# Kernel optimization log

Measured on AMD Instinct MI355X. Metric: run time of the kernel, lower is better.

The kernel has to match this reference:

```python
import jax, jax.numpy as jnp
import numpy as np

D_MODEL = 1024
N_HEADS = 16
DEPTH = D_MODEL // N_HEADS
B, S = 2, 2048


def setup_inputs() -> dict:
    key = jax.random.key(0)
    ks = jax.random.split(key, 11)
    scale = 1.0 / np.sqrt(D_MODEL)
    return {
        "q": jax.random.normal(ks[0], (B, S, D_MODEL), jnp.float32),
        "k": jax.random.normal(ks[1], (B, S, D_MODEL), jnp.float32),
        "v": jax.random.normal(ks[2], (B, S, D_MODEL), jnp.float32),
        "wq": jax.random.normal(ks[3], (D_MODEL, D_MODEL), jnp.float32) * scale,
        "bq": jnp.zeros((D_MODEL,), jnp.float32),
        "wk": jax.random.normal(ks[4], (D_MODEL, D_MODEL), jnp.float32) * scale,
        "bk": jnp.zeros((D_MODEL,), jnp.float32),
        "wv": jax.random.normal(ks[5], (D_MODEL, D_MODEL), jnp.float32) * scale,
        "bv": jnp.zeros((D_MODEL,), jnp.float32),
        "wo": jax.random.normal(ks[6], (D_MODEL, D_MODEL), jnp.float32) * scale,
        "bo": jnp.zeros((D_MODEL,), jnp.float32),
    }


def _mha(q, k, v, wq, bq, wk, bk, wv, bv, wo, bo):
    b, s, _ = q.shape
    # separate QKV projections
    qh = (q @ wq + bq).reshape(b, s, N_HEADS, DEPTH).transpose(0, 2, 1, 3)  # [b,h,s,d]
    kh = (k @ wk + bk).reshape(b, s, N_HEADS, DEPTH).transpose(0, 2, 1, 3)
    vh = (v @ wv + bv).reshape(b, s, N_HEADS, DEPTH).transpose(0, 2, 1, 3)
    # keras.layers.Attention default: UNSCALED dot-product scores, causal mask
    scores = jnp.einsum("bhqd,bhkd->bhqk", qh, kh)  # [b,h,s,s]
    causal = jnp.tril(jnp.ones((s, s), bool))
    scores = jnp.where(causal, scores, jnp.float32(-1e9))
    attn = jax.nn.softmax(scores, axis=-1)
    out = jnp.einsum("bhqk,bhkd->bhqd", attn, vh)  # [b,h,s,d]
    out = out.transpose(0, 2, 1, 3).reshape(b, s, D_MODEL)
    return out @ wo + bo


def reference(q, k, v, wq, bq, wk, bk, wv, bv, wo, bo):
    return _mha(q, k, v, wq, bq, wk, bk, wv, bv, wo, bo)
```

## Files before the change

kernel.cpp:

```cpp
#include <hip/hip_runtime.h>
#include <stdint.h>

#define AS1q __attribute__((address_space(1)))
#define AS3q __attribute__((address_space(3)))

typedef unsigned short US;
typedef __bf16 bf16x8 __attribute__((ext_vector_type(8)));
typedef float f32x4 __attribute__((ext_vector_type(4)));

__device__ __forceinline__ US f2bf(float f) {
  union { float f; uint32_t u; } c; c.f = f;
  uint32_t u = c.u;
  return (US)((u + 0x7fffu + ((u >> 16) & 1u)) >> 16);
}

__device__ __forceinline__ float bf2f(US h) {
  union { uint32_t u; float f; } c; c.u = ((uint32_t)h) << 16; return c.f;
}

__device__ __forceinline__ bf16x8 asb(uint4 u) {
  union { uint4 u; bf16x8 b; } c; c.u = u; return c.b;
}

__device__ __forceinline__ void gload16(const void* g, void* l) {
  __builtin_amdgcn_global_load_lds((AS1q void*)(void*)g, (AS3q void*)l, 16, 0, 0);
}

__global__ void prep_kernel(const float* __restrict__ q, const float* __restrict__ k,
                            const float* __restrict__ v,
                            const float* __restrict__ w0, const float* __restrict__ w1,
                            const float* __restrict__ w2, const float* __restrict__ w3,
                            US* __restrict__ qb, US* __restrict__ kb, US* __restrict__ vb,
                            US* __restrict__ t0, US* __restrict__ t1,
                            US* __restrict__ t2, US* __restrict__ t3) {
  __shared__ US T[64 * 68];
  const int bx = blockIdx.x;
  const int t = threadIdx.x;
  if (bx < 6144) {
    const int ten = bx >> 11, chunk = bx & 2047;
    const float* s; US* d;
    if (ten == 0)      { s = q; d = qb; }
    else if (ten == 1) { s = k; d = kb; }
    else               { s = v; d = vb; }
    int i = (chunk * 256 + t) * 8;
    float4 f0 = *(const float4*)&s[i];
    float4 f1 = *(const float4*)&s[i + 4];
    ushort4 u0, u1;
    u0.x = f2bf(f0.x); u0.y = f2bf(f0.y); u0.z = f2bf(f0.z); u0.w = f2bf(f0.w);
    u1.x = f2bf(f1.x); u1.y = f2bf(f1.y); u1.z = f2bf(f1.z); u1.w = f2bf(f1.w);
    *(ushort4*)&d[i] = u0;
    *(ushort4*)&d[i + 4] = u1;
    return;
  }
  const int idx = bx - 6144;
  const int wsel = idx >> 8, rem = idx & 255;
  const int n0 = (rem & 15) * 64, k0 = (rem >> 4) * 64;
  const float* W; US* Wt;
  if (wsel == 0)      { W = w0; Wt = t0; }
  else if (wsel == 1) { W = w1; Wt = t1; }
  else if (wsel == 2) { W = w2; Wt = t2; }
  else                { W = w3; Wt = t3; }
#pragma unroll
  for (int it = 0; it < 4; ++it) {
    int p = t + it * 256;
    int row = p >> 4, c4 = (p & 15) * 4;
    float4 f = *(const float4*)&W[(k0 + row) * 1024 + n0 + c4];
    ushort4 u;
    u.x = f2bf(f.x); u.y = f2bf(f.y); u.z = f2bf(f.z); u.w = f2bf(f.w);
    *(ushort4*)&T[row * 68 + c4] = u;
  }
  __syncthreads();
#pragma unroll
  for (int it = 0; it < 4; ++it) {
    int p = t + it * 256;
    int rn = p >> 4, ck = (p & 15) * 4;
    ushort4 o;
    o.x = T[(ck + 0) * 68 + rn];
    o.y = T[(ck + 1) * 68 + rn];
    o.z = T[(ck + 2) * 68 + rn];
    o.w = T[(ck + 3) * 68 + rn];
    *(ushort4*)&Wt[(n0 + rn) * 1024 + k0 + ck] = o;
  }
}

__device__ __forceinline__ void gemm_core(const US* A, const US* Wt,
                                          int m0, int n0, US* As, US* Bs,
                                          f32x4 acc[4][4]) {
  const int tid = threadIdx.x;
  const int wave = tid >> 6, lane = tid & 63;
  const int quad = lane >> 4, l16 = lane & 15;
  const int wm = wave >> 1, wn = wave & 1;
#pragma unroll
  for (int i = 0; i < 4; ++i)
#pragma unroll
    for (int j = 0; j < 4; ++j) acc[i][j] = (f32x4)0.0f;
  const int p = wave * 64 + lane;
  const int arow0 = p >> 2, koff = (p & 3) * 8;
  for (int k0 = 0; k0 < 1024; k0 += 32) {
    gload16(A + (m0 + arow0) * 1024 + k0 + koff, As + wave * 512);
    gload16(A + (m0 + arow0 + 64) * 1024 + k0 + koff, As + 2048 + wave * 512);
    gload16(Wt + (n0 + arow0) * 1024 + k0 + koff, Bs + wave * 512);
    gload16(Wt + (n0 + arow0 + 64) * 1024 + k0 + koff, Bs + 2048 + wave * 512);
    __syncthreads();
    uint4 af[4], bf_[4];
#pragma unroll
    for (int mt = 0; mt < 4; ++mt)
      af[mt] = *(const uint4*)&As[(wm * 64 + mt * 16 + l16) * 32 + quad * 8];
#pragma unroll
    for (int nt = 0; nt < 4; ++nt)
      bf_[nt] = *(const uint4*)&Bs[(wn * 64 + nt * 16 + l16) * 32 + quad * 8];
#pragma unroll
    for (int mt = 0; mt < 4; ++mt)
#pragma unroll
      for (int nt = 0; nt < 4; ++nt)
        acc[mt][nt] = __builtin_amdgcn_mfma_f32_16x16x32_bf16(asb(af[mt]), asb(bf_[nt]),
                                                              acc[mt][nt], 0, 0, 0);
    __syncthreads();
  }
}

__global__ __launch_bounds__(256, 2) void gemm_qkv_kernel(
    const US* __restrict__ qb, const US* __restrict__ kb, const US* __restrict__ vb,
    const US* __restrict__ wqT, const US* __restrict__ wkT, const US* __restrict__ wvT,
    const float* __restrict__ bq, const float* __restrict__ bk, const float* __restrict__ bv,
    US* __restrict__ qh, US* __restrict__ kh, US* __restrict__ vt) {
  __shared__ __align__(16) US As[4096], Bs[4096];
  const US* A; const US* W; const float* bias;
  if (blockIdx.z == 0)      { A = qb; W = wqT; bias = bq; }
  else if (blockIdx.z == 1) { A = kb; W = wkT; bias = bk; }
  else                      { A = vb; W = wvT; bias = bv; }
  const int m0 = blockIdx.x * 128, n0 = blockIdx.y * 128;
  f32x4 acc[4][4];
  gemm_core(A, W, m0, n0, As, Bs, acc);
  const int tid = threadIdx.x, wave = tid >> 6, lane = tid & 63;
  const int quad = lane >> 4, l16 = lane & 15;
  const int wm = wave >> 1, wn = wave & 1;
  if (blockIdx.z == 2) {
#pragma unroll
    for (int nt = 0; nt < 4; ++nt) {
      int n = n0 + wn * 64 + nt * 16 + l16;
      float bval = bias[n];
      int hh = n >> 6, d = n & 63;
#pragma unroll
      for (int mt = 0; mt < 4; ++mt) {
        int m = m0 + wm * 64 + mt * 16 + quad * 4;
        int bb = m >> 11, s = m & 2047;
        ushort4 u;
        u.x = f2bf(acc[mt][nt][0] + bval);
        u.y = f2bf(acc[mt][nt][1] + bval);
        u.z = f2bf(acc[mt][nt][2] + bval);
        u.w = f2bf(acc[mt][nt][3] + bval);
        *(ushort4*)&vt[((bb * 16 + hh) * 64 + d) * 2048 + s] = u;
      }
    }
  } else {
    US* O = (blockIdx.z == 0) ? qh : kh;
#pragma unroll
    for (int nt = 0; nt < 4; ++nt) {
      int n = n0 + wn * 64 + nt * 16 + l16;
      float bval = bias[n];
      int hh = n >> 6, d = n & 63;
#pragma unroll
      for (int mt = 0; mt < 4; ++mt) {
#pragma unroll
        for (int r = 0; r < 4; ++r) {
          int m = m0 + wm * 64 + mt * 16 + quad * 4 + r;
          int bb = m >> 11, s = m & 2047;
          O[((bb * 16 + hh) * 2048 + s) * 64 + d] = f2bf(acc[mt][nt][r] + bval);
        }
      }
    }
  }
}

__global__ __launch_bounds__(256, 2) void gemm_out_kernel(
    const US* __restrict__ ao, const US* __restrict__ woT,
    const float* __restrict__ bo, float* __restrict__ out) {
  __shared__ __align__(16) US As[4096], Bs[4096];
  const int m0 = blockIdx.x * 128, n0 = blockIdx.y * 128;
  f32x4 acc[4][4];
  gemm_core(ao, woT, m0, n0, As, Bs, acc);
  const int tid = threadIdx.x, wave = tid >> 6, lane = tid & 63;
  const int quad = lane >> 4, l16 = lane & 15;
  const int wm = wave >> 1, wn = wave & 1;
#pragma unroll
  for (int nt = 0; nt < 4; ++nt) {
    int n = n0 + wn * 64 + nt * 16 + l16;
    float bval = bo[n];
#pragma unroll
    for (int mt = 0; mt < 4; ++mt) {
#pragma unroll
      for (int r = 0; r < 4; ++r) {
        int m = m0 + wm * 64 + mt * 16 + quad * 4 + r;
        out[m * 1024 + n] = acc[mt][nt][r] + bval;
      }
    }
  }
}

__global__ __launch_bounds__(512, 4) void attn_kernel(
    const US* __restrict__ qh, const US* __restrict__ kh,
    const US* __restrict__ vt, US* __restrict__ aout) {
  __shared__ __align__(16) US Qs[4096];
  __shared__ __align__(16) US Ks[2][4096];
  __shared__ __align__(16) US Vs[2][4096];
  __shared__ __align__(16) US Ps[8 * 640];
  __shared__ float Oex[4][16][68];
  __shared__ float lEx[4][16];
  const int tid = threadIdx.x;
  const int wave = tid >> 6, lane = tid & 63;
  const int quad = lane >> 4, l16 = lane & 15;
  const int w_m = wave & 3, w_k = wave >> 2;
  const int bh = blockIdx.x;
  const int b = bh >> 4, h = bh & 15;
  const int pair = blockIdx.y;

  const int srow = tid >> 3, sc = (tid & 7) ^ (srow & 7);

  const US* gkb = kh + (size_t)bh * 2048 * 64;
  const US* gvb = vt + (size_t)bh * 64 * 2048;

  for (int half = 0; half < 2; ++half) {
    const int qt = half ? (31 - pair) : pair;
    const int q0 = qt * 64;
    __syncthreads();
    {
      const US* gq = qh + ((size_t)bh * 2048 + q0) * 64;
      gload16(gq + srow * 64 + sc * 8, Qs + wave * 512);
      gload16(gkb + srow * 64 + sc * 8, Ks[0] + wave * 512);
      gload16(gvb + srow * 2048 + sc * 8, Vs[0] + wave * 512);
    }
    __syncthreads();

    const int qrow = w_m * 16 + l16;
    uint4 aq0 = *(const uint4*)&Qs[qrow * 64 + (((0 * 4 + quad) ^ (qrow & 7)) * 8)];
    uint4 aq1 = *(const uint4*)&Qs[qrow * 64 + (((1 * 4 + quad) ^ (qrow & 7)) * 8)];

    float l_part[4] = {0.f, 0.f, 0.f, 0.f};
    f32x4 Of[4];
#pragma unroll
    for (int nt = 0; nt < 4; ++nt) Of[nt] = (f32x4)0.0f;
    const int grow_base = q0 + w_m * 16 + quad * 4;

    US* pw = Ps + wave * 640;

    for (int kt = 0; kt <= qt; ++kt) {
      const int cb = kt & 1;
      if (kt) __syncthreads();
      if (kt < qt) {
        const US* gk = gkb + (kt + 1) * 64 * 64;
        const US* gv = gvb + (kt + 1) * 64;
        gload16(gk + srow * 64 + sc * 8, Ks[cb ^ 1] + wave * 512);
        gload16(gv + srow * 2048 + sc * 8, Vs[cb ^ 1] + wave * 512);
      }
      const US* Kc = Ks[cb];
      const US* Vc = Vs[cb];

      f32x4 sacc[2];
      sacc[0] = (f32x4)0.0f; sacc[1] = (f32x4)0.0f;
#pragma unroll
      for (int nt = 0; nt < 2; ++nt) {
        int krow = w_k * 32 + nt * 16 + l16;
        uint4 bk0 = *(const uint4*)&Kc[krow * 64 + ((quad ^ (krow & 7)) * 8)];
        sacc[nt] = __builtin_amdgcn_mfma_f32_16x16x32_bf16(asb(aq0), asb(bk0), sacc[nt], 0, 0, 0);
      }
#pragma unroll
      for (int nt = 0; nt < 2; ++nt) {
        int krow = w_k * 32 + nt * 16 + l16;
        uint4 bk1 = *(const uint4*)&Kc[krow * 64 + (((4 + quad) ^ (krow & 7)) * 8)];
        sacc[nt] = __builtin_amdgcn_mfma_f32_16x16x32_bf16(asb(aq1), asb(bk1), sacc[nt], 0, 0, 0);
      }
      if (kt == qt) {
#pragma unroll
        for (int nt = 0; nt < 2; ++nt) {
          int gcol = q0 + w_k * 32 + nt * 16 + l16;
#pragma unroll
          for (int r = 0; r < 4; ++r)
            if (gcol > grow_base + r) sacc[nt][r] = -1e30f;
        }
      }

#pragma unroll
      for (int nt = 0; nt < 2; ++nt) {
#pragma unroll
        for (int r = 0; r < 4; ++r) {
          float e = __expf(sacc[nt][r]);
          US hb = f2bf(e);
          l_part[r] += bf2f(hb);
          pw[(quad * 4 + r) * 40 + nt * 16 + l16] = hb;
        }
      }
      __asm__ volatile("s_waitcnt lgkmcnt(0)" ::: "memory");

      uint4 ap = *(const uint4*)&pw[l16 * 40 + quad * 8];
#pragma unroll
      for (int nt = 0; nt < 4; ++nt) {
        int vrow = nt * 16 + l16;
        uint4 bv_ = *(const uint4*)&Vc[vrow * 64 + (((w_k * 4 + quad) ^ (vrow & 7)) * 8)];
        Of[nt] = __builtin_amdgcn_mfma_f32_16x16x32_bf16(asb(ap), asb(bv_), Of[nt], 0, 0, 0);
      }
    }

    float l_red[4];
#pragma unroll
    for (int r = 0; r < 4; ++r) {
      float s = l_part[r];
#pragma unroll
      for (int off = 1; off < 16; off <<= 1) s += __shfl_xor(s, off, 64);
      l_red[r] = s;
    }

    __syncthreads();
    if (w_k == 1) {
#pragma unroll
      for (int nt = 0; nt < 4; ++nt)
#pragma unroll
        for (int r = 0; r < 4; ++r)
          Oex[w_m][quad * 4 + r][nt * 16 + l16] = Of[nt][r];
      if (l16 == 0) {
#pragma unroll
        for (int r = 0; r < 4; ++r) lEx[w_m][quad * 4 + r] = l_red[r];
      }
    }
    __syncthreads();
    if (w_k == 0) {
#pragma unroll
      for (int r = 0; r < 4; ++r) {
        float ltot = l_red[r] + lEx[w_m][quad * 4 + r];
        float inv = 1.0f / ltot;
        int row = grow_base + r;
#pragma unroll
        for (int nt = 0; nt < 4; ++nt) {
          float o = Of[nt][r] + Oex[w_m][quad * 4 + r][nt * 16 + l16];
          aout[((size_t)b * 2048 + row) * 1024 + h * 64 + nt * 16 + l16] = f2bf(o * inv);
        }
      }
    }
  }
}

extern "C" void kernel_launch(void* const* d_in, const int* in_sizes, int n_in,
                              void* d_out, int out_size, void* d_ws, size_t ws_size,
                              hipStream_t stream) {
  const float* q  = (const float*)d_in[0];
  const float* k  = (const float*)d_in[1];
  const float* v  = (const float*)d_in[2];
  const float* wq = (const float*)d_in[3];
  const float* bq = (const float*)d_in[4];
  const float* wk = (const float*)d_in[5];
  const float* bk = (const float*)d_in[6];
  const float* wv = (const float*)d_in[7];
  const float* bv = (const float*)d_in[8];
  const float* wo = (const float*)d_in[9];
  const float* bo = (const float*)d_in[10];
  float* out = (float*)d_out;

  char* ws = (char*)d_ws;
  const size_t MB = 1024 * 1024;
  US* qb  = (US*)(ws + 0 * MB);
  US* kb  = (US*)(ws + 8 * MB);
  US* vb  = (US*)(ws + 16 * MB);
  US* wqT = (US*)(ws + 24 * MB);
  US* wkT = (US*)(ws + 26 * MB);
  US* wvT = (US*)(ws + 28 * MB);
  US* woT = (US*)(ws + 30 * MB);
  US* qh  = (US*)(ws + 32 * MB);
  US* kh  = (US*)(ws + 40 * MB);
  US* vt  = (US*)(ws + 48 * MB);
  US* ao  = (US*)(ws + 56 * MB);

  prep_kernel<<<7168, 256, 0, stream>>>(q, k, v, wq, wk, wv, wo,
                                        qb, kb, vb, wqT, wkT, wvT, woT);
  gemm_qkv_kernel<<<dim3(32, 8, 3), 256, 0, stream>>>(qb, kb, vb, wqT, wkT, wvT,
                                                      bq, bk, bv, qh, kh, vt);
  attn_kernel<<<dim3(32, 16), 512, 0, stream>>>(qh, kh, vt, ao);
  gemm_out_kernel<<<dim3(32, 8), 256, 0, stream>>>(ao, woT, bo, out);
}
```

Before: 219.7 us.

## Rebalance causal attention tiles across more blocks and shrink shared memory

Attention work is repacked from 16 paired query tiles per head into 24 groups. Long tiles run alone and short tiles are paired so the per-block work is more even. Q/P staging and the cross-wave reduction buffers now share one LDS union, and launch bounds rise to 6 blocks per SM, aiming at higher occupancy. The V projection epilogue swaps MFMA operands so the transposed vt stores become contiguous along the sequence. Softmax now uses packed bf16 conversion and sums the fp32 exponentials instead of the rounded ones, which slightly changes the normaliser numerics.

```diff
diff --git a/kernel.cpp b/kernel.cpp
--- a/kernel.cpp
+++ b/kernel.cpp
@@ -7,15 +7,13 @@
 typedef unsigned short US;
 typedef __bf16 bf16x8 __attribute__((ext_vector_type(8)));
 typedef float f32x4 __attribute__((ext_vector_type(4)));
+typedef float f32x2 __attribute__((ext_vector_type(2)));
+typedef __bf16 bf16x2 __attribute__((ext_vector_type(2)));
 
 __device__ __forceinline__ US f2bf(float f) {
   union { float f; uint32_t u; } c; c.f = f;
   uint32_t u = c.u;
   return (US)((u + 0x7fffu + ((u >> 16) & 1u)) >> 16);
-}
-
-__device__ __forceinline__ float bf2f(US h) {
-  union { uint32_t u; float f; } c; c.u = ((uint32_t)h) << 16; return c.f;
 }
 
 __device__ __forceinline__ bf16x8 asb(uint4 u) {
@@ -83,6 +81,7 @@
   }
 }
 
+template <bool SWAP>
 __device__ __forceinline__ void gemm_core(const US* A, const US* Wt,
                                           int m0, int n0, US* As, US* Bs,
                                           f32x4 acc[4][4]) {
@@ -110,11 +109,16 @@
     for (int nt = 0; nt < 4; ++nt)
       bf_[nt] = *(const uint4*)&Bs[(wn * 64 + nt * 16 + l16) * 32 + quad * 8];
 #pragma unroll
-    for (int mt = 0; mt < 4; ++mt)
-#pragma unroll
-      for (int nt = 0; nt < 4; ++nt)
-        acc[mt][nt] = __builtin_amdgcn_mfma_f32_16x16x32_bf16(asb(af[mt]), asb(bf_[nt]),
-                                                              acc[mt][nt], 0, 0, 0);
+    for (int i = 0; i < 4; ++i)
+#pragma unroll
+      for (int j = 0; j < 4; ++j) {
+        if (SWAP)
+          acc[i][j] = __builtin_amdgcn_mfma_f32_16x16x32_bf16(asb(bf_[i]), asb(af[j]),
+                                                              acc[i][j], 0, 0, 0);
+        else
+          acc[i][j] = __builtin_amdgcn_mfma_f32_16x16x32_bf16(asb(af[i]), asb(bf_[j]),
+                                                              acc[i][j], 0, 0, 0);
+      }
     __syncthreads();
   }
 }
@@ -130,30 +134,31 @@
   else if (blockIdx.z == 1) { A = kb; W = wkT; bias = bk; }
   else                      { A = vb; W = wvT; bias = bv; }
   const int m0 = blockIdx.x * 128, n0 = blockIdx.y * 128;
-  f32x4 acc[4][4];
-  gemm_core(A, W, m0, n0, As, Bs, acc);
   const int tid = threadIdx.x, wave = tid >> 6, lane = tid & 63;
   const int quad = lane >> 4, l16 = lane & 15;
   const int wm = wave >> 1, wn = wave & 1;
+  f32x4 acc[4][4];
   if (blockIdx.z == 2) {
+    gemm_core<true>(A, W, m0, n0, As, Bs, acc);
 #pragma unroll
     for (int nt = 0; nt < 4; ++nt) {
-      int n = n0 + wn * 64 + nt * 16 + l16;
-      float bval = bias[n];
-      int hh = n >> 6, d = n & 63;
-#pragma unroll
-      for (int mt = 0; mt < 4; ++mt) {
-        int m = m0 + wm * 64 + mt * 16 + quad * 4;
-        int bb = m >> 11, s = m & 2047;
-        ushort4 u;
-        u.x = f2bf(acc[mt][nt][0] + bval);
-        u.y = f2bf(acc[mt][nt][1] + bval);
-        u.z = f2bf(acc[mt][nt][2] + bval);
-        u.w = f2bf(acc[mt][nt][3] + bval);
-        *(ushort4*)&vt[((bb * 16 + hh) * 64 + d) * 2048 + s] = u;
+      int dg = n0 + wn * 64 + nt * 16 + quad * 4;
+#pragma unroll
+      for (int r = 0; r < 4; ++r) {
+        int d = dg + r;
+        float bval = bias[d];
+        int hh = d >> 6, dd = d & 63;
+#pragma unroll
+        for (int mt = 0; mt < 4; ++mt) {
+          int sg = m0 + wm * 64 + mt * 16;
+          int bb = sg >> 11, ss = sg & 2047;
+          vt[(((size_t)bb * 16 + hh) * 64 + dd) * 2048 + ss + l16] =
+              f2bf(acc[nt][mt][r] + bval);
+        }
       }
     }
   } else {
+    gemm_core<false>(A, W, m0, n0, As, Bs, acc);
     US* O = (blockIdx.z == 0) ? qh : kh;
 #pragma unroll
     for (int nt = 0; nt < 4; ++nt) {
@@ -179,7 +184,7 @@
   __shared__ __align__(16) US As[4096], Bs[4096];
   const int m0 = blockIdx.x * 128, n0 = blockIdx.y * 128;
   f32x4 acc[4][4];
-  gemm_core(ao, woT, m0, n0, As, Bs, acc);
+  gemm_core<false>(ao, woT, m0, n0, As, Bs, acc);
   const int tid = threadIdx.x, wave = tid >> 6, lane = tid & 63;
   const int quad = lane >> 4, l16 = lane & 15;
   const int wm = wave >> 1, wn = wave & 1;
@@ -198,43 +203,49 @@
   }
 }
 
-__global__ __launch_bounds__(512, 4) void attn_kernel(
+__global__ __launch_bounds__(512, 6) void attn_kernel(
     const US* __restrict__ qh, const US* __restrict__ kh,
     const US* __restrict__ vt, US* __restrict__ aout) {
-  __shared__ __align__(16) US Qs[4096];
   __shared__ __align__(16) US Ks[2][4096];
   __shared__ __align__(16) US Vs[2][4096];
-  __shared__ __align__(16) US Ps[8 * 640];
-  __shared__ float Oex[4][16][68];
-  __shared__ float lEx[4][16];
+  __shared__ __align__(16) union UU {
+    struct { US Qs[4096]; US Ps[8 * 640]; } s;
+    struct { float Oex[4][16][65]; float lEx[4][16]; } e;
+  } u;
   const int tid = threadIdx.x;
   const int wave = tid >> 6, lane = tid & 63;
   const int quad = lane >> 4, l16 = lane & 15;
   const int w_m = wave & 3, w_k = wave >> 2;
   const int bh = blockIdx.x;
   const int b = bh >> 4, h = bh & 15;
-  const int pair = blockIdx.y;
+  const int g = blockIdx.y;
+
+  int t0, t1;
+  if (g < 11)      { t0 = 31 - g; t1 = -1; }
+  else if (g < 19) { int j = g - 11; t0 = 16 - j; t1 = j; }
+  else if (g < 23) { t0 = 17 + (g - 19); t1 = -1; }
+  else             { t0 = 8; t1 = -1; }
 
   const int srow = tid >> 3, sc = (tid & 7) ^ (srow & 7);
-
   const US* gkb = kh + (size_t)bh * 2048 * 64;
   const US* gvb = vt + (size_t)bh * 64 * 2048;
 
-  for (int half = 0; half < 2; ++half) {
-    const int qt = half ? (31 - pair) : pair;
+  for (int ei = 0; ei < 2; ++ei) {
+    const int qt = ei ? t1 : t0;
+    if (qt < 0) break;
     const int q0 = qt * 64;
     __syncthreads();
     {
       const US* gq = qh + ((size_t)bh * 2048 + q0) * 64;
-      gload16(gq + srow * 64 + sc * 8, Qs + wave * 512);
+      gload16(gq + srow * 64 + sc * 8, u.s.Qs + wave * 512);
       gload16(gkb + srow * 64 + sc * 8, Ks[0] + wave * 512);
       gload16(gvb + srow * 2048 + sc * 8, Vs[0] + wave * 512);
     }
     __syncthreads();
 
     const int qrow = w_m * 16 + l16;
-    uint4 aq0 = *(const uint4*)&Qs[qrow * 64 + (((0 * 4 + quad) ^ (qrow & 7)) * 8)];
-    uint4 aq1 = *(const uint4*)&Qs[qrow * 64 + (((1 * 4 + quad) ^ (qrow & 7)) * 8)];
+    uint4 aq0 = *(const uint4*)&u.s.Qs[qrow * 64 + ((quad ^ (qrow & 7)) * 8)];
+    uint4 aq1 = *(const uint4*)&u.s.Qs[qrow * 64 + (((4 + quad) ^ (qrow & 7)) * 8)];
 
     float l_part[4] = {0.f, 0.f, 0.f, 0.f};
     f32x4 Of[4];
@@ -242,7 +253,7 @@
     for (int nt = 0; nt < 4; ++nt) Of[nt] = (f32x4)0.0f;
     const int grow_base = q0 + w_m * 16 + quad * 4;
 
-    US* pw = Ps + wave * 640;
+    US* pw = u.s.Ps + wave * 640;
 
     for (int kt = 0; kt <= qt; ++kt) {
       const int cb = kt & 1;
@@ -283,11 +294,16 @@
 #pragma unroll
       for (int nt = 0; nt < 2; ++nt) {
 #pragma unroll
-        for (int r = 0; r < 4; ++r) {
-          float e = __expf(sacc[nt][r]);
-          US hb = f2bf(e);
-          l_part[r] += bf2f(hb);
-          pw[(quad * 4 + r) * 40 + nt * 16 + l16] = hb;
+        for (int r = 0; r < 4; r += 2) {
+          float e0 = __expf(sacc[nt][r]);
+          float e1 = __expf(sacc[nt][r + 1]);
+          l_part[r] += e0;
+          l_part[r + 1] += e1;
+          f32x2 fv; fv[0] = e0; fv[1] = e1;
+          bf16x2 bv2 = __builtin_convertvector(fv, bf16x2);
+          union { bf16x2 b; ushort2 u; } cc; cc.b = bv2;
+          pw[(quad * 4 + r) * 40 + nt * 16 + l16] = cc.u.x;
+          pw[(quad * 4 + r + 1) * 40 + nt * 16 + l16] = cc.u.y;
         }
       }
       __asm__ volatile("s_waitcnt lgkmcnt(0)" ::: "memory");
@@ -316,22 +332,22 @@
       for (int nt = 0; nt < 4; ++nt)
 #pragma unroll
         for (int r = 0; r < 4; ++r)
-          Oex[w_m][quad * 4 + r][nt * 16 + l16] = Of[nt][r];
+          u.e.Oex[w_m][quad * 4 + r][nt * 16 + l16] = Of[nt][r];
       if (l16 == 0) {
 #pragma unroll
-        for (int r = 0; r < 4; ++r) lEx[w_m][quad * 4 + r] = l_red[r];
+        for (int r = 0; r < 4; ++r) u.e.lEx[w_m][quad * 4 + r] = l_red[r];
       }
     }
     __syncthreads();
     if (w_k == 0) {
 #pragma unroll
       for (int r = 0; r < 4; ++r) {
-        float ltot = l_red[r] + lEx[w_m][quad * 4 + r];
+        float ltot = l_red[r] + u.e.lEx[w_m][quad * 4 + r];
         float inv = 1.0f / ltot;
         int row = grow_base + r;
 #pragma unroll
         for (int nt = 0; nt < 4; ++nt) {
-          float o = Of[nt][r] + Oex[w_m][quad * 4 + r][nt * 16 + l16];
+          float o = Of[nt][r] + u.e.Oex[w_m][quad * 4 + r][nt * 16 + l16];
           aout[((size_t)b * 2048 + row) * 1024 + h * 64 + nt * 16 + l16] = f2bf(o * inv);
         }
       }
@@ -373,6 +389,6 @@
                                         qb, kb, vb, wqT, wkT, wvT, woT);
   gemm_qkv_kernel<<<dim3(32, 8, 3), 256, 0, stream>>>(qb, kb, vb, wqT, wkT, wvT,
                                                       bq, bk, bv, qh, kh, vt);
-  attn_kernel<<<dim3(32, 16), 512, 0, stream>>>(qh, kh, vt, ao);
+  attn_kernel<<<dim3(32, 24), 512, 0, stream>>>(qh, kh, vt, ao);
   gemm_out_kernel<<<dim3(32, 8), 256, 0, stream>>>(ao, woT, bo, out);
 }
```

Result: faster. 212.6 us (-3.2%).
